# Optimization experiments

Measured on AMD Instinct MI355X. Metric: run time of the kernel, lower is better.

The kernel has to match this reference:

```python
import jax, jax.numpy as jnp
import numpy as np

B, N, T, F, H, HEADS, E, EDIM, P = 4, 1000, 8, 64, 64, 4, 16000, 16, 5
NEG_SLOPE = 0.2


def _seg_softmax(e, seg, n):
    # segment softmax over destination nodes; every segment is nonempty (self-loops)
    m = jax.ops.segment_max(e, seg, num_segments=n)
    ex = jnp.exp(e - m[seg])
    s = jax.ops.segment_sum(ex, seg, num_segments=n)
    return ex / s[seg]


def _gat(x, ei, W, a_src, a_dst, b):
    # PyG GATConv with concat=False (mean over heads), self-loops already in ei
    n = x.shape[0]
    heads, hh = a_src.shape
    h = (x @ W).reshape(n, heads, hh)                       # [N, heads, H]
    asrc = (h * a_src).sum(-1)                              # [N, heads]
    adst = (h * a_dst).sum(-1)
    src, dst = ei[0], ei[1]
    e = jax.nn.leaky_relu(asrc[src] + adst[dst], NEG_SLOPE)  # [E2, heads]
    alpha = _seg_softmax(e, dst, n)
    out = jax.ops.segment_sum(alpha[:, :, None] * h[src], dst, num_segments=n)
    return out.mean(1) + b                                   # [N, H]


def _gru_cell(x, h, Wih, Whh, bih, bhh):
    gi = x @ Wih.T + bih
    gh = h @ Whh.T + bhh
    i_r, i_z, i_n = jnp.split(gi, 3, axis=-1)
    h_r, h_z, h_n = jnp.split(gh, 3, axis=-1)
    r = jax.nn.sigmoid(i_r + h_r)
    z = jax.nn.sigmoid(i_z + h_z)
    nn_ = jnp.tanh(i_n + r * h_n)
    return (1.0 - z) * nn_ + z * h


def setup_inputs() -> dict:
    key = jax.random.key(0)
    ks = jax.random.split(key, 20)
    rn = lambda k, shp, s: (jax.random.normal(k, shp, jnp.float32) * s)
    inp = {}
    inp['x'] = jax.random.normal(ks[0], (B, N, T, F), jnp.float32)
    inp['edge_index_seq'] = jax.random.randint(ks[1], (B, T, 2, E), 0, N)
    inp['edge_feat_seq'] = jax.random.normal(ks[2], (B, T, E, EDIM), jnp.float32)
    inp['W1'] = rn(ks[3], (F, HEADS * H), 1 / np.sqrt(F))
    inp['att_src1'] = rn(ks[4], (HEADS, H), 1 / np.sqrt(H))
    inp['att_dst1'] = rn(ks[5], (HEADS, H), 1 / np.sqrt(H))
    inp['b1'] = jnp.zeros((H,), jnp.float32)
    inp['W2'] = rn(ks[6], (H, HEADS * H), 1 / np.sqrt(H))
    inp['att_src2'] = rn(ks[7], (HEADS, H), 1 / np.sqrt(H))
    inp['att_dst2'] = rn(ks[8], (HEADS, H), 1 / np.sqrt(H))
    inp['b2'] = jnp.zeros((H,), jnp.float32)
    inp['edge_W'] = rn(ks[9], (EDIM, H), 1 / np.sqrt(EDIM))
    inp['edge_b'] = jnp.zeros((H,), jnp.float32)
    inp['Wih0'] = rn(ks[10], (3 * H, H), 1 / np.sqrt(H))
    inp['Whh0'] = rn(ks[11], (3 * H, H), 1 / np.sqrt(H))
    inp['bih0'] = jnp.zeros((3 * H,), jnp.float32)
    inp['bhh0'] = jnp.zeros((3 * H,), jnp.float32)
    inp['Wih1'] = rn(ks[12], (3 * H, H), 1 / np.sqrt(H))
    inp['Whh1'] = rn(ks[13], (3 * H, H), 1 / np.sqrt(H))
    inp['bih1'] = jnp.zeros((3 * H,), jnp.float32)
    inp['bhh1'] = jnp.zeros((3 * H,), jnp.float32)
    inp['pW1'] = rn(ks[14], (H, H), 1 / np.sqrt(H))
    inp['pb1'] = jnp.zeros((H,), jnp.float32)
    inp['pW2'] = rn(ks[15], (H, 2 * P), 1 / np.sqrt(H))
    inp['pb2'] = jnp.zeros((2 * P,), jnp.float32)
    return inp


def reference(x, edge_index_seq, edge_feat_seq, W1, att_src1, att_dst1, b1,
              W2, att_src2, att_dst2, b2, edge_W, edge_b,
              Wih0, Whh0, bih0, bhh0, Wih1, Whh1, bih1, bhh1,
              pW1, pb1, pW2, pb2):
    Bs, Ns, Ts, Fs = x.shape
    G = Bs * Ts
    # [B,N,T,F] -> [B*T, N, F] (graph per (b,t))
    xg = x.transpose(0, 2, 1, 3).reshape(G, Ns, Fs)
    ei = edge_index_seq.reshape(G, 2, -1)
    # add self-loops (PyG GATConv default)
    sl = jnp.broadcast_to(jnp.arange(Ns), (G, 2, Ns))
    ei = jnp.concatenate([ei, sl], axis=-1)

    def per_graph(xt, e):
        h = jax.nn.relu(_gat(xt, e, W1, att_src1, att_dst1, b1))
        return _gat(h, e, W2, att_src2, att_dst2, b2)

    h = jax.vmap(per_graph)(xg, ei)                         # [G, N, H]
    Hd = h.shape[-1]
    # note: original computes edge_embedding(edge_feat) but never uses it (dead code)
    h = h.reshape(Bs, Ts, Ns, Hd).transpose(0, 2, 1, 3).reshape(Bs * Ns, Ts, Hd)
    xs = h.transpose(1, 0, 2)                               # [T, B*N, H]
    h0 = jnp.zeros((Bs * Ns, Hd), x.dtype)

    def step(carry, xt):
        h1, h2 = carry
        h1n = _gru_cell(xt, h1, Wih0, Whh0, bih0, bhh0)
        h2n = _gru_cell(h1n, h2, Wih1, Whh1, bih1, bhh1)
        return (h1n, h2n), None

    (_, hT), _ = jax.lax.scan(step, (h0, h0), xs)           # hT: [B*N, H]
    mid = jax.nn.relu(hT @ pW1 + pb1)
    pred = mid @ pW2 + pb2                                  # [B*N, 2P]
    return pred.reshape(Bs, Ns, P, 2)
```

## Files before the change

### kernel.cpp

```cpp
#include <hip/hip_runtime.h>
#include <math.h>

#define BB 4
#define NN 1000
#define TT 8
#define FF 64
#define HH 64
#define NHEADS 4
#define EE 16000
#define E2 17000
#define GG (BB*TT)
#define GN (GG*NN)
#define NROWS (BB*NN)

typedef __attribute__((ext_vector_type(8))) short bf16x8;
typedef __attribute__((ext_vector_type(4))) float f32x4;

__device__ __forceinline__ float sigmoidf_(float x) {
    return 1.f / (1.f + __expf(-x));
}
__device__ __forceinline__ float tanhf_(float x) {
    x = fminf(fmaxf(x, -15.f), 15.f);
    float e = __expf(2.f * x);
    return (e - 1.f) / (e + 1.f);
}
__device__ __forceinline__ float leaky_(float x) {
    return (x > 0.f) ? x : 0.2f * x;
}
__device__ __forceinline__ ushort bf16_rne(float v) {
    uint b = __float_as_uint(v);
    return (ushort)((b + 0x7FFF + ((b >> 16) & 1)) >> 16);
}

__global__ void count_edges(const int* __restrict__ ei, int* __restrict__ counts) {
    int g = blockIdx.y;
    int e = blockIdx.x * 256 + threadIdx.x;
    if (e >= E2) return;
    int dst;
    if (e < EE) dst = ei[(size_t)g * 2 * EE + EE + e];
    else        dst = e - EE;
    atomicAdd(&counts[g * NN + dst], 1);
}

__global__ __launch_bounds__(256) void scan_offsets_pg(const int* __restrict__ counts,
                                                       int* __restrict__ offs) {
    __shared__ int tot[256];
    int g = blockIdx.x;
    int tid = threadIdx.x;
    int base = tid * 4;
    int c0 = 0, c1 = 0, c2 = 0, c3 = 0;
    if (base < NN) {
        int4 v = *(const int4*)(counts + (size_t)g * NN + base);
        c0 = v.x; c1 = v.y; c2 = v.z; c3 = v.w;
    }
    int s = c0 + c1 + c2 + c3;
    tot[tid] = s;
    __syncthreads();
    for (int off = 1; off < 256; off <<= 1) {
        int y = (tid >= off) ? tot[tid - off] : 0;
        __syncthreads();
        tot[tid] += y;
        __syncthreads();
    }
    int run = g * E2 + tot[tid] - s;
    if (base < NN) {
        int4 o;
        o.x = run; run += c0;
        o.y = run; run += c1;
        o.z = run; run += c2;
        o.w = run;
        *(int4*)(offs + (size_t)g * NN + base) = o;
    }
    if (g == 0 && tid == 0) offs[GN] = GG * E2;
}

__global__ void scatter_edges(const int* __restrict__ ei, const int* __restrict__ offs,
                              int* __restrict__ cursor, int* __restrict__ csr) {
    int g = blockIdx.y;
    int e = blockIdx.x * 256 + threadIdx.x;
    if (e >= E2) return;
    int src, dst;
    if (e < EE) {
        src = ei[(size_t)g * 2 * EE + e];
        dst = ei[(size_t)g * 2 * EE + EE + e];
    } else {
        src = dst = e - EE;
    }
    int i = g * NN + dst;
    int pos = offs[i] + atomicAdd(&cursor[i], 1);
    csr[pos] = src;
}

#define PIN64_(arr)                                        \
    _Pragma("unroll")                                      \
    for (int _pi = 0; _pi < 64; ++_pi)                     \
        asm volatile("" : "+v"((arr)[_pi]));


template <int MODE>
__global__ __launch_bounds__(256) void xprep(
    const float* __restrict__ in, ushort* __restrict__ ap) {
    int g = blockIdx.x / 63, mt = blockIdx.x % 63;
    int tid = threadIdx.x;
    int xq = tid >> 7, kb = (tid >> 6) & 1, row = (tid >> 2) & 15, koct = tid & 3;
    int n = mt * 16 + row;
    int f0 = kb * 32 + koct * 8;
    float v[8];
    if (n < NN) {
        const float* xr;
        if (MODE == 0) {
            int b = g / TT, t = g % TT;
            xr = in + (((size_t)(b * NN + n) * TT + t) * FF);
        } else {
            xr = in + ((size_t)(g * NN + n) * FF);
        }
        float4 a = *(const float4*)(xr + f0);
        float4 c = *(const float4*)(xr + f0 + 4);
        v[0] = a.x; v[1] = a.y; v[2] = a.z; v[3] = a.w;
        v[4] = c.x; v[5] = c.y; v[6] = c.z; v[7] = c.w;
    } else {
#pragma unroll
        for (int j = 0; j < 8; ++j) v[j] = 0.f;
    }
    ushort o[8];
#pragma unroll
    for (int j = 0; j < 8; ++j) {
        ushort h = bf16_rne(v[j]);
        if (xq == 0) o[j] = h;
        else {
            float hf = __uint_as_float(((uint)h) << 16);
            o[j] = bf16_rne(v[j] - hf);
        }
    }
    size_t off = (size_t)(g * 63 + mt) * 2048
               + ((size_t)((xq * 2 + kb) * 16 + row) * 4 + koct) * 8;
    uint4 ow;
    ow.x = (uint)o[0] | ((uint)o[1] << 16);
    ow.y = (uint)o[2] | ((uint)o[3] << 16);
    ow.z = (uint)o[4] | ((uint)o[5] << 16);
    ow.w = (uint)o[6] | ((uint)o[7] << 16);
    *(uint4*)(ap + off) = ow;
}

__global__ __launch_bounds__(64) void wprep(
    const float* __restrict__ W1, const float* __restrict__ W2,
    ushort* __restrict__ B1, ushort* __restrict__ B2) {
    int blk = blockIdx.x;
    const float* W = (blk >> 6) ? W2 : W1;
    ushort* Bp = (blk >> 6) ? B2 : B1;
    int r = blk & 63;
    int wq = r >> 5, kb = (r >> 4) & 1, nt = r & 15;
    int tid = threadIdx.x;
    int col = tid >> 2, koct = tid & 3;
    int c = nt * 16 + col;
    ushort o[8];
#pragma unroll
    for (int j = 0; j < 8; ++j) {
        int k = kb * 32 + koct * 8 + j;
        float v = W[k * 256 + c];
        ushort h = bf16_rne(v);
        if (wq == 0) o[j] = h;
        else {
            float hf = __uint_as_float(((uint)h) << 16);
            o[j] = bf16_rne(v - hf);
        }
    }
    size_t off = (((size_t)((wq * 2 + kb) * 16 + nt) * 16 + col) * 4 + koct) * 8;
    uint4 ow;
    ow.x = (uint)o[0] | ((uint)o[1] << 16);
    ow.y = (uint)o[2] | ((uint)o[3] << 16);
    ow.z = (uint)o[4] | ((uint)o[5] << 16);
    ow.w = (uint)o[6] | ((uint)o[7] << 16);
    *(uint4*)(Bp + off) = ow;
}

__global__ __launch_bounds__(256) void gat_mfma(
    const ushort* __restrict__ ap, const ushort* __restrict__ bp,
    const float* __restrict__ att_s, const float* __restrict__ att_d,
    float* __restrict__ hlin, float* __restrict__ asrc, float* __restrict__ adst) {
    int g = blockIdx.x >> 4, band = blockIdx.x & 15;
    int tid = threadIdx.x;
    int w = tid >> 6, lane = tid & 63;
    int mt = band * 4 + w;
    if (mt >= 63) return;
    int lo = lane & 15, hi = lane >> 4;

    const ushort* abase = ap + (size_t)(g * 63 + mt) * 2048;
    size_t foff = ((size_t)(lo * 4 + hi)) * 8;
    bf16x8 Ah0 = *(const bf16x8*)(abase + 0 * 512 + foff);
    bf16x8 Ah1 = *(const bf16x8*)(abase + 1 * 512 + foff);
    bf16x8 Al0 = *(const bf16x8*)(abase + 2 * 512 + foff);
    bf16x8 Al1 = *(const bf16x8*)(abase + 3 * 512 + foff);

    f32x4 acc[16];
#pragma unroll
    for (int i = 0; i < 16; ++i) acc[i] = (f32x4){0.f, 0.f, 0.f, 0.f};

#pragma unroll
    for (int nt = 0; nt < 16; ++nt) {
        const ushort* bb = bp + (size_t)nt * 512 + foff;
        bf16x8 Bh0 = *(const bf16x8*)(bb + 0 * 8192);
        bf16x8 Bh1 = *(const bf16x8*)(bb + 1 * 8192);
        bf16x8 Bl0 = *(const bf16x8*)(bb + 2 * 8192);
        bf16x8 Bl1 = *(const bf16x8*)(bb + 3 * 8192);
        acc[nt] = __builtin_amdgcn_mfma_f32_16x16x32_bf16(Ah0, Bh0, acc[nt], 0, 0, 0);
        acc[nt] = __builtin_amdgcn_mfma_f32_16x16x32_bf16(Ah1, Bh1, acc[nt], 0, 0, 0);
        acc[nt] = __builtin_amdgcn_mfma_f32_16x16x32_bf16(Ah0, Bl0, acc[nt], 0, 0, 0);
        acc[nt] = __builtin_amdgcn_mfma_f32_16x16x32_bf16(Ah1, Bl1, acc[nt], 0, 0, 0);
        acc[nt] = __builtin_amdgcn_mfma_f32_16x16x32_bf16(Al0, Bh0, acc[nt], 0, 0, 0);
        acc[nt] = __builtin_amdgcn_mfma_f32_16x16x32_bf16(Al1, Bh1, acc[nt], 0, 0, 0);
        acc[nt] = __builtin_amdgcn_mfma_f32_16x16x32_bf16(Al0, Bl0, acc[nt], 0, 0, 0);
        acc[nt] = __builtin_amdgcn_mfma_f32_16x16x32_bf16(Al1, Bl1, acc[nt], 0, 0, 0);
    }

    float s1[4][4], s2[4][4];
#pragma unroll
    for (int r = 0; r < 4; ++r)
#pragma unroll
        for (int h = 0; h < 4; ++h) { s1[r][h] = 0.f; s2[r][h] = 0.f; }

#pragma unroll
    for (int nt = 0; nt < 16; ++nt) {
        int c = nt * 16 + lo;
        int head = nt >> 2;
        int slot = ((c & 63) << 2) + head;
        float as = att_s[c];
        float ad = att_d[c];
#pragma unroll
        for (int reg = 0; reg < 4; ++reg) {
            int n = mt * 16 + hi * 4 + reg;
            float v = acc[nt][reg];
            if (n < NN)
                hlin[((size_t)(g * NN + n) << 8) + slot] = v;
            s1[reg][head] += v * as;
            s2[reg][head] += v * ad;
        }
    }
#pragma unroll
    for (int off = 1; off < 16; off <<= 1) {
#pragma unroll
        for (int reg = 0; reg < 4; ++reg)
#pragma unroll
            for (int h = 0; h < 4; ++h) {
                s1[reg][h] += __shfl_xor(s1[reg][h], off, 64);
                s2[reg][h] += __shfl_xor(s2[reg][h], off, 64);
            }
    }
    if (lo == 0) {
#pragma unroll
        for (int reg = 0; reg < 4; ++reg) {
            int n = mt * 16 + hi * 4 + reg;
            if (n < NN) {
#pragma unroll
                for (int h = 0; h < 4; ++h) {
                    asrc[(size_t)(g * NN + n) * NHEADS + h] = s1[reg][h];
                    adst[(size_t)(g * NN + n) * NHEADS + h] = s2[reg][h];
                }
            }
        }
    }
}

__global__ __launch_bounds__(256) void gat_edge(
    const float* __restrict__ hlin, const float* __restrict__ asrc,
    const float* __restrict__ adst, const int* __restrict__ offs,
    const int* __restrict__ csr, const float* __restrict__ bias,
    float* __restrict__ out, int do_relu) {
    __shared__ float pbuf[4][64][4];
    __shared__ int   sbuf[4][64];
    __shared__ int   degs[4];
    int tid = threadIdx.x;
    int lane = tid & 63, w = tid >> 6;
    int B = blockIdx.x;
    int x = B & 7, j = B >> 3;
    int graph = x + 8 * (j / 250);
    int node = graph * NN + ((j % 250) << 2) + w;
    int beg = offs[node], end = offs[node + 1];
    int deg = end - beg;
    if (lane == 0) degs[w] = deg;
    __syncthreads();
    int maxdeg = max(max(degs[0], degs[1]), max(degs[2], degs[3]));
    int nchunk = (maxdeg + 63) >> 6;

    float4 ad = *(const float4*)(adst + (size_t)node * 4);
    const float* asrc_g = asrc + (size_t)graph * NN * 4;
    const float* hg = hlin + ((size_t)graph * NN << 8);

    float4 acc = make_float4(0.f, 0.f, 0.f, 0.f);
    float4 ssum = make_float4(0.f, 0.f, 0.f, 0.f);
    for (int c = 0; c < nchunk; ++c) {
        int e0 = beg + (c << 6);
        int myedge = e0 + lane;
        float4 p = make_float4(0.f, 0.f, 0.f, 0.f);
        int src = 0;
        if (myedge < end) {
            src = csr[myedge];
            float4 a = *(const float4*)(asrc_g + (size_t)src * 4);
            p.x = __expf(leaky_(a.x + ad.x));
            p.y = __expf(leaky_(a.y + ad.y));
            p.z = __expf(leaky_(a.z + ad.z));
            p.w = __expf(leaky_(a.w + ad.w));
        }
        float4 t = p;
#pragma unroll
        for (int off = 1; off < 64; off <<= 1) {
            t.x += __shfl_xor(t.x, off, 64);
            t.y += __shfl_xor(t.y, off, 64);
            t.z += __shfl_xor(t.z, off, 64);
            t.w += __shfl_xor(t.w, off, 64);
        }
        ssum.x += t.x; ssum.y += t.y; ssum.z += t.z; ssum.w += t.w;
        *(float4*)&pbuf[w][lane][0] = p;
        sbuf[w][lane] = src;
        __syncthreads();
        int cnt = end - e0;
        if (cnt > 64) cnt = 64;
        int cnt8 = (cnt + 7) & ~7;
        for (int e = 0; e < cnt8; e += 8) {
            float4 p0 = *(const float4*)&pbuf[w][e + 0][0];
            float4 p1 = *(const float4*)&pbuf[w][e + 1][0];
            float4 p2 = *(const float4*)&pbuf[w][e + 2][0];
            float4 p3 = *(const float4*)&pbuf[w][e + 3][0];
            float4 p4 = *(const float4*)&pbuf[w][e + 4][0];
            float4 p5 = *(const float4*)&pbuf[w][e + 5][0];
            float4 p6 = *(const float4*)&pbuf[w][e + 6][0];
            float4 p7 = *(const float4*)&pbuf[w][e + 7][0];
            int s0 = sbuf[w][e + 0], s1 = sbuf[w][e + 1];
            int s2 = sbuf[w][e + 2], s3 = sbuf[w][e + 3];
            int s4 = sbuf[w][e + 4], s5 = sbuf[w][e + 5];
            int s6 = sbuf[w][e + 6], s7 = sbuf[w][e + 7];
            int lo = lane << 2;
            float4 h0 = *(const float4*)(hg + (((size_t)s0) << 8) + lo);
            float4 h1 = *(const float4*)(hg + (((size_t)s1) << 8) + lo);
            float4 h2 = *(const float4*)(hg + (((size_t)s2) << 8) + lo);
            float4 h3 = *(const float4*)(hg + (((size_t)s3) << 8) + lo);
            float4 h4 = *(const float4*)(hg + (((size_t)s4) << 8) + lo);
            float4 h5 = *(const float4*)(hg + (((size_t)s5) << 8) + lo);
            float4 h6 = *(const float4*)(hg + (((size_t)s6) << 8) + lo);
            float4 h7 = *(const float4*)(hg + (((size_t)s7) << 8) + lo);
            acc.x = fmaf(p0.x, h0.x, acc.x); acc.y = fmaf(p0.y, h0.y, acc.y);
            acc.z = fmaf(p0.z, h0.z, acc.z); acc.w = fmaf(p0.w, h0.w, acc.w);
            acc.x = fmaf(p1.x, h1.x, acc.x); acc.y = fmaf(p1.y, h1.y, acc.y);
            acc.z = fmaf(p1.z, h1.z, acc.z); acc.w = fmaf(p1.w, h1.w, acc.w);
            acc.x = fmaf(p2.x, h2.x, acc.x); acc.y = fmaf(p2.y, h2.y, acc.y);
            acc.z = fmaf(p2.z, h2.z, acc.z); acc.w = fmaf(p2.w, h2.w, acc.w);
            acc.x = fmaf(p3.x, h3.x, acc.x); acc.y = fmaf(p3.y, h3.y, acc.y);
            acc.z = fmaf(p3.z, h3.z, acc.z); acc.w = fmaf(p3.w, h3.w, acc.w);
            acc.x = fmaf(p4.x, h4.x, acc.x); acc.y = fmaf(p4.y, h4.y, acc.y);
            acc.z = fmaf(p4.z, h4.z, acc.z); acc.w = fmaf(p4.w, h4.w, acc.w);
            acc.x = fmaf(p5.x, h5.x, acc.x); acc.y = fmaf(p5.y, h5.y, acc.y);
            acc.z = fmaf(p5.z, h5.z, acc.z); acc.w = fmaf(p5.w, h5.w, acc.w);
            acc.x = fmaf(p6.x, h6.x, acc.x); acc.y = fmaf(p6.y, h6.y, acc.y);
            acc.z = fmaf(p6.z, h6.z, acc.z); acc.w = fmaf(p6.w, h6.w, acc.w);
            acc.x = fmaf(p7.x, h7.x, acc.x); acc.y = fmaf(p7.y, h7.y, acc.y);
            acc.z = fmaf(p7.z, h7.z, acc.z); acc.w = fmaf(p7.w, h7.w, acc.w);
        }
        __syncthreads();
    }
    float o = 0.25f * (acc.x / ssum.x + acc.y / ssum.y + acc.z / ssum.z + acc.w / ssum.w)
            + bias[lane];
    if (do_relu) o = fmaxf(o, 0.f);
    out[((size_t)node << 6) + lane] = o;
}

template <int MODE>
__global__ __launch_bounds__(192, 4) void gru_gi(
    const float* __restrict__ in, const float* __restrict__ Wih,
    const float* __restrict__ bih, float* __restrict__ giseq) {
    const int ROWS = 10;
    int j = threadIdx.x;
    float wrow[64];
#pragma unroll
    for (int f4 = 0; f4 < 16; ++f4) {
        float4 w = *(const float4*)(Wih + (size_t)j * 64 + f4 * 4);
        wrow[4 * f4 + 0] = w.x; wrow[4 * f4 + 1] = w.y;
        wrow[4 * f4 + 2] = w.z; wrow[4 * f4 + 3] = w.w;
    }
    PIN64_(wrow)
    float bj = bih[j];
    int q0 = blockIdx.x * ROWS;
    int t = q0 / NROWS;
    int r0 = q0 - t * NROWS;
    for (int rr = 0; rr < ROWS; rr += 2) {
        const float *xa, *xb;
        if (MODE == 0) {
            int ra = r0 + rr, rb = ra + 1;
            int ba = ra / NN, na = ra - ba * NN;
            int bb2 = rb / NN, nb = rb - bb2 * NN;
            xa = in + (((size_t)(ba * TT + t) * NN + na) << 6);
            xb = in + (((size_t)(bb2 * TT + t) * NN + nb) << 6);
        } else {
            xa = in + ((size_t)(q0 + rr) << 6);
            xb = xa + 64;
        }
        float acca = bj, accb = bj;
#pragma unroll
        for (int f4 = 0; f4 < 16; ++f4) {
            float4 a4 = *(const float4*)(xa + f4 * 4);
            float4 b4 = *(const float4*)(xb + f4 * 4);
            acca = fmaf(a4.x, wrow[4 * f4 + 0], acca);
            acca = fmaf(a4.y, wrow[4 * f4 + 1], acca);
            acca = fmaf(a4.z, wrow[4 * f4 + 2], acca);
            acca = fmaf(a4.w, wrow[4 * f4 + 3], acca);
            accb = fmaf(b4.x, wrow[4 * f4 + 0], accb);
            accb = fmaf(b4.y, wrow[4 * f4 + 1], accb);
            accb = fmaf(b4.z, wrow[4 * f4 + 2], accb);
            accb = fmaf(b4.w, wrow[4 * f4 + 3], accb);
        }
        giseq[(size_t)(q0 + rr) * 192 + j] = acca;
        giseq[(size_t)(q0 + rr + 1) * 192 + j] = accb;
    }
}

template <int LAYER>
__global__ __launch_bounds__(128) void gru_rec(
    const float* __restrict__ giseq, const float* __restrict__ Whh,
    const float* __restrict__ bhh, float* __restrict__ outseq) {
    __shared__ float hs[4][64];
    int tid = threadIdx.x;
    int ch = tid & 63, w = tid >> 6;
    float wr[64], wz[64], wn[64];
#pragma unroll
    for (int k4 = 0; k4 < 16; ++k4) {
        float4 a = *(const float4*)(Whh + (size_t)ch * 64 + k4 * 4);
        float4 b = *(const float4*)(Whh + (size_t)(64 + ch) * 64 + k4 * 4);
        float4 c = *(const float4*)(Whh + (size_t)(128 + ch) * 64 + k4 * 4);
        wr[4*k4+0] = a.x; wr[4*k4+1] = a.y; wr[4*k4+2] = a.z; wr[4*k4+3] = a.w;
        wz[4*k4+0] = b.x; wz[4*k4+1] = b.y; wz[4*k4+2] = b.z; wz[4*k4+3] = b.w;
        wn[4*k4+0] = c.x; wn[4*k4+1] = c.y; wn[4*k4+2] = c.z; wn[4*k4+3] = c.w;
    }
    float br = bhh[ch], bz = bhh[64 + ch], bn = bhh[128 + ch];
    int row0 = blockIdx.x * 4 + w * 2;
    float hprev[2];
#pragma unroll
    for (int r = 0; r < 2; ++r) { hs[w * 2 + r][ch] = 0.f; hprev[r] = 0.f; }

    for (int t = 0; t < TT; ++t) {
#pragma unroll
        for (int r = 0; r < 2; ++r) {
            int row = row0 + r;
            const float* gp = giseq + ((size_t)(t * NROWS + row)) * 192;
            float gir = gp[ch], giz = gp[64 + ch], gin = gp[128 + ch];
            float ar = br, az = bz, an = bn;
#pragma unroll
            for (int k4 = 0; k4 < 16; ++k4) {
                float4 h4 = *(const float4*)&hs[w * 2 + r][k4 * 4];
                ar = fmaf(h4.x, wr[4*k4+0], ar); ar = fmaf(h4.y, wr[4*k4+1], ar);
                ar = fmaf(h4.z, wr[4*k4+2], ar); ar = fmaf(h4.w, wr[4*k4+3], ar);
                az = fmaf(h4.x, wz[4*k4+0], az); az = fmaf(h4.y, wz[4*k4+1], az);
                az = fmaf(h4.z, wz[4*k4+2], az); az = fmaf(h4.w, wz[4*k4+3], az);
                an = fmaf(h4.x, wn[4*k4+0], an); an = fmaf(h4.y, wn[4*k4+1], an);
                an = fmaf(h4.z, wn[4*k4+2], an); an = fmaf(h4.w, wn[4*k4+3], an);
            }
            float rg = sigmoidf_(gir + ar);
            float zg = sigmoidf_(giz + az);
            float ng = tanhf_(gin + rg * an);
            float hnew = (1.f - zg) * ng + zg * hprev[r];
            hprev[r] = hnew;
            hs[w * 2 + r][ch] = hnew;
            if (LAYER == 0)
                outseq[(((size_t)(t * NROWS + row)) << 6) + ch] = hnew;
        }
    }
    if (LAYER == 1) {
#pragma unroll
        for (int r = 0; r < 2; ++r)
            outseq[(((size_t)(row0 + r)) << 6) + ch] = hprev[r];
    }
}

__global__ __launch_bounds__(64) void mlp_head(
    const float* __restrict__ hT, const float* __restrict__ pW1,
    const float* __restrict__ pb1, const float* __restrict__ pW2,
    const float* __restrict__ pb2, float* __restrict__ out) {
    int r = blockIdx.x, lane = threadIdx.x;
    __shared__ float hrow[64];
    __shared__ float mid[64];
    hrow[lane] = hT[((size_t)r << 6) + lane];
    __syncthreads();
    float acc = pb1[lane];
#pragma unroll
    for (int k = 0; k < 64; ++k) acc = fmaf(hrow[k], pW1[k * 64 + lane], acc);
    mid[lane] = fmaxf(acc, 0.f);
    __syncthreads();
    if (lane < 10) {
        float o = pb2[lane];
#pragma unroll
        for (int k = 0; k < 64; ++k) o = fmaf(mid[k], pW2[k * 10 + lane], o);
        out[(size_t)r * 10 + lane] = o;
    }
}

extern "C" void kernel_launch(void* const* d_in, const int* in_sizes, int n_in,
                              void* d_out, int out_size, void* d_ws, size_t ws_size,
                              hipStream_t stream) {
    (void)in_sizes; (void)n_in; (void)out_size; (void)ws_size;
    const float* x    = (const float*)d_in[0];
    const int*   ei   = (const int*)d_in[1];
    const float* W1   = (const float*)d_in[3];
    const float* as1  = (const float*)d_in[4];
    const float* ad1  = (const float*)d_in[5];
    const float* b1   = (const float*)d_in[6];
    const float* W2   = (const float*)d_in[7];
    const float* as2  = (const float*)d_in[8];
    const float* ad2  = (const float*)d_in[9];
    const float* b2   = (const float*)d_in[10];
    const float* Wih0 = (const float*)d_in[13];
    const float* Whh0 = (const float*)d_in[14];
    const float* bih0 = (const float*)d_in[15];
    const float* bhh0 = (const float*)d_in[16];
    const float* Wih1 = (const float*)d_in[17];
    const float* Whh1 = (const float*)d_in[18];
    const float* bih1 = (const float*)d_in[19];
    const float* bhh1 = (const float*)d_in[20];
    const float* pW1  = (const float*)d_in[21];
    const float* pb1  = (const float*)d_in[22];
    const float* pW2  = (const float*)d_in[23];
    const float* pb2  = (const float*)d_in[24];
    float* out = (float*)d_out;

    char* ws = (char*)d_ws;
    float* hlin  = (float*)(ws + 0);
    float* giseq = hlin;
    float* asrc  = (float*)(ws + 32768000);
    float* hT    = asrc;
    float* adst  = (float*)(ws + 33280000);
    float* gat1  = (float*)(ws + 33792000);
    float* h1seq = gat1;
    float* gat2  = (float*)(ws + 41984000);
    ushort* Apack = (ushort*)(ws + 41984000);
    int* counts  = (int*)(ws + 50176000);
    int* cursor  = (int*)(ws + 50304000);
    int* offs    = (int*)(ws + 50432000);
    int* csr     = (int*)(ws + 50560256);
    ushort* Bp1  = (ushort*)(ws + 52736256);
    ushort* Bp2  = (ushort*)(ws + 52801792);

    hipMemsetAsync(counts, 0, 2 * GN * sizeof(int), stream);

    dim3 egrid((E2 + 255) / 256, GG);
    count_edges<<<egrid, 256, 0, stream>>>(ei, counts);
    scan_offsets_pg<<<GG, 256, 0, stream>>>(counts, offs);
    scatter_edges<<<egrid, 256, 0, stream>>>(ei, offs, cursor, csr);

    wprep<<<128, 64, 0, stream>>>(W1, W2, Bp1, Bp2);

    xprep<0><<<GG * 63, 256, 0, stream>>>(x, Apack);
    gat_mfma<<<GG * 16, 256, 0, stream>>>(Apack, Bp1, as1, ad1, hlin, asrc, adst);
    gat_edge<<<GN / 4, 256, 0, stream>>>(hlin, asrc, adst, offs, csr, b1, gat1, 1);
    xprep<1><<<GG * 63, 256, 0, stream>>>(gat1, Apack);
    gat_mfma<<<GG * 16, 256, 0, stream>>>(Apack, Bp2, as2, ad2, hlin, asrc, adst);
    gat_edge<<<GN / 4, 256, 0, stream>>>(hlin, asrc, adst, offs, csr, b2, gat2, 0);

    gru_gi<0><<<3200, 192, 0, stream>>>(gat2, Wih0, bih0, giseq);
    gru_rec<0><<<1000, 128, 0, stream>>>(giseq, Whh0, bhh0, h1seq);
    gru_gi<1><<<3200, 192, 0, stream>>>(h1seq, Wih1, bih1, giseq);
    gru_rec<1><<<1000, 128, 0, stream>>>(giseq, Whh1, bhh1, hT);

    mlp_head<<<NROWS, 64, 0, stream>>>(hT, pW1, pb1, pW2, pb2, out);
}
```

Measured before the change: 423.9 us.

## Fuse bf16 hi/lo input split into GAT MFMA kernel and split columns across waves

Removes the separate xprep pass that packed inputs into split bf16 hi/lo tiles; each GAT projection kernel now loads the fp32 rows directly and builds the A fragments in registers. The block grows to 512 threads so that two waves share each row tile, each computing half the output columns (two heads). This drops two kernel launches and the global round trip for the packed buffer, and halves the accumulator registers per wave. In exchange, the fp32 input is read by both wave halves, and the per-lane loads are less coalesced than the prepacked layout.

```diff
diff --git a/kernel.cpp b/kernel.cpp
--- a/kernel.cpp
+++ b/kernel.cpp
@@ -96,51 +96,6 @@
     for (int _pi = 0; _pi < 64; ++_pi)                     \
         asm volatile("" : "+v"((arr)[_pi]));
 
-
-template <int MODE>
-__global__ __launch_bounds__(256) void xprep(
-    const float* __restrict__ in, ushort* __restrict__ ap) {
-    int g = blockIdx.x / 63, mt = blockIdx.x % 63;
-    int tid = threadIdx.x;
-    int xq = tid >> 7, kb = (tid >> 6) & 1, row = (tid >> 2) & 15, koct = tid & 3;
-    int n = mt * 16 + row;
-    int f0 = kb * 32 + koct * 8;
-    float v[8];
-    if (n < NN) {
-        const float* xr;
-        if (MODE == 0) {
-            int b = g / TT, t = g % TT;
-            xr = in + (((size_t)(b * NN + n) * TT + t) * FF);
-        } else {
-            xr = in + ((size_t)(g * NN + n) * FF);
-        }
-        float4 a = *(const float4*)(xr + f0);
-        float4 c = *(const float4*)(xr + f0 + 4);
-        v[0] = a.x; v[1] = a.y; v[2] = a.z; v[3] = a.w;
-        v[4] = c.x; v[5] = c.y; v[6] = c.z; v[7] = c.w;
-    } else {
-#pragma unroll
-        for (int j = 0; j < 8; ++j) v[j] = 0.f;
-    }
-    ushort o[8];
-#pragma unroll
-    for (int j = 0; j < 8; ++j) {
-        ushort h = bf16_rne(v[j]);
-        if (xq == 0) o[j] = h;
-        else {
-            float hf = __uint_as_float(((uint)h) << 16);
-            o[j] = bf16_rne(v[j] - hf);
-        }
-    }
-    size_t off = (size_t)(g * 63 + mt) * 2048
-               + ((size_t)((xq * 2 + kb) * 16 + row) * 4 + koct) * 8;
-    uint4 ow;
-    ow.x = (uint)o[0] | ((uint)o[1] << 16);
-    ow.y = (uint)o[2] | ((uint)o[3] << 16);
-    ow.z = (uint)o[4] | ((uint)o[5] << 16);
-    ow.w = (uint)o[6] | ((uint)o[7] << 16);
-    *(uint4*)(ap + off) = ow;
-}
 
 __global__ __launch_bounds__(64) void wprep(
     const float* __restrict__ W1, const float* __restrict__ W2,
@@ -174,88 +129,119 @@
     *(uint4*)(Bp + off) = ow;
 }
 
-__global__ __launch_bounds__(256) void gat_mfma(
-    const ushort* __restrict__ ap, const ushort* __restrict__ bp,
+template <int MODE>
+__global__ __launch_bounds__(512, 4) void gat_mfma(
+    const float* __restrict__ in, const ushort* __restrict__ bp,
     const float* __restrict__ att_s, const float* __restrict__ att_d,
     float* __restrict__ hlin, float* __restrict__ asrc, float* __restrict__ adst) {
     int g = blockIdx.x >> 4, band = blockIdx.x & 15;
     int tid = threadIdx.x;
     int w = tid >> 6, lane = tid & 63;
-    int mt = band * 4 + w;
+    int mt = band * 4 + (w & 3);
+    int half = w >> 2;
     if (mt >= 63) return;
     int lo = lane & 15, hi = lane >> 4;
-
-    const ushort* abase = ap + (size_t)(g * 63 + mt) * 2048;
+    int n = mt * 16 + lo;
+
+    float xv[16];
+    if (n < NN) {
+        const float* xr;
+        if (MODE == 0) {
+            int b = g / TT, t = g % TT;
+            xr = in + (((size_t)(b * NN + n) * TT + t) * FF);
+        } else {
+            xr = in + ((size_t)(g * NN + n) * FF);
+        }
+        float4 a0 = *(const float4*)(xr + hi * 8);
+        float4 a1 = *(const float4*)(xr + hi * 8 + 4);
+        float4 b0 = *(const float4*)(xr + 32 + hi * 8);
+        float4 b1 = *(const float4*)(xr + 32 + hi * 8 + 4);
+        xv[0] = a0.x; xv[1] = a0.y; xv[2]  = a0.z; xv[3]  = a0.w;
+        xv[4] = a1.x; xv[5] = a1.y; xv[6]  = a1.z; xv[7]  = a1.w;
+        xv[8] = b0.x; xv[9] = b0.y; xv[10] = b0.z; xv[11] = b0.w;
+        xv[12] = b1.x; xv[13] = b1.y; xv[14] = b1.z; xv[15] = b1.w;
+    } else {
+#pragma unroll
+        for (int j = 0; j < 16; ++j) xv[j] = 0.f;
+    }
+    bf16x8 Ah0, Ah1, Al0, Al1;
+#pragma unroll
+    for (int j = 0; j < 8; ++j) {
+        ushort h0 = bf16_rne(xv[j]);
+        Ah0[j] = (short)h0;
+        Al0[j] = (short)bf16_rne(xv[j] - __uint_as_float(((uint)h0) << 16));
+        ushort h1 = bf16_rne(xv[8 + j]);
+        Ah1[j] = (short)h1;
+        Al1[j] = (short)bf16_rne(xv[8 + j] - __uint_as_float(((uint)h1) << 16));
+    }
+
     size_t foff = ((size_t)(lo * 4 + hi)) * 8;
-    bf16x8 Ah0 = *(const bf16x8*)(abase + 0 * 512 + foff);
-    bf16x8 Ah1 = *(const bf16x8*)(abase + 1 * 512 + foff);
-    bf16x8 Al0 = *(const bf16x8*)(abase + 2 * 512 + foff);
-    bf16x8 Al1 = *(const bf16x8*)(abase + 3 * 512 + foff);
-
-    f32x4 acc[16];
-#pragma unroll
-    for (int i = 0; i < 16; ++i) acc[i] = (f32x4){0.f, 0.f, 0.f, 0.f};
-
-#pragma unroll
-    for (int nt = 0; nt < 16; ++nt) {
+    f32x4 acc[8];
+#pragma unroll
+    for (int i = 0; i < 8; ++i) acc[i] = (f32x4){0.f, 0.f, 0.f, 0.f};
+
+#pragma unroll
+    for (int q = 0; q < 8; ++q) {
+        int nt = half * 8 + q;
         const ushort* bb = bp + (size_t)nt * 512 + foff;
         bf16x8 Bh0 = *(const bf16x8*)(bb + 0 * 8192);
         bf16x8 Bh1 = *(const bf16x8*)(bb + 1 * 8192);
         bf16x8 Bl0 = *(const bf16x8*)(bb + 2 * 8192);
         bf16x8 Bl1 = *(const bf16x8*)(bb + 3 * 8192);
-        acc[nt] = __builtin_amdgcn_mfma_f32_16x16x32_bf16(Ah0, Bh0, acc[nt], 0, 0, 0);
-        acc[nt] = __builtin_amdgcn_mfma_f32_16x16x32_bf16(Ah1, Bh1, acc[nt], 0, 0, 0);
-        acc[nt] = __builtin_amdgcn_mfma_f32_16x16x32_bf16(Ah0, Bl0, acc[nt], 0, 0, 0);
-        acc[nt] = __builtin_amdgcn_mfma_f32_16x16x32_bf16(Ah1, Bl1, acc[nt], 0, 0, 0);
-        acc[nt] = __builtin_amdgcn_mfma_f32_16x16x32_bf16(Al0, Bh0, acc[nt], 0, 0, 0);
-        acc[nt] = __builtin_amdgcn_mfma_f32_16x16x32_bf16(Al1, Bh1, acc[nt], 0, 0, 0);
-        acc[nt] = __builtin_amdgcn_mfma_f32_16x16x32_bf16(Al0, Bl0, acc[nt], 0, 0, 0);
-        acc[nt] = __builtin_amdgcn_mfma_f32_16x16x32_bf16(Al1, Bl1, acc[nt], 0, 0, 0);
-    }
-
-    float s1[4][4], s2[4][4];
-#pragma unroll
-    for (int r = 0; r < 4; ++r)
-#pragma unroll
-        for (int h = 0; h < 4; ++h) { s1[r][h] = 0.f; s2[r][h] = 0.f; }
-
-#pragma unroll
-    for (int nt = 0; nt < 16; ++nt) {
+        acc[q] = __builtin_amdgcn_mfma_f32_16x16x32_bf16(Ah0, Bh0, acc[q], 0, 0, 0);
+        acc[q] = __builtin_amdgcn_mfma_f32_16x16x32_bf16(Ah1, Bh1, acc[q], 0, 0, 0);
+        acc[q] = __builtin_amdgcn_mfma_f32_16x16x32_bf16(Ah0, Bl0, acc[q], 0, 0, 0);
+        acc[q] = __builtin_amdgcn_mfma_f32_16x16x32_bf16(Ah1, Bl1, acc[q], 0, 0, 0);
+        acc[q] = __builtin_amdgcn_mfma_f32_16x16x32_bf16(Al0, Bh0, acc[q], 0, 0, 0);
+        acc[q] = __builtin_amdgcn_mfma_f32_16x16x32_bf16(Al1, Bh1, acc[q], 0, 0, 0);
+        acc[q] = __builtin_amdgcn_mfma_f32_16x16x32_bf16(Al0, Bl0, acc[q], 0, 0, 0);
+        acc[q] = __builtin_amdgcn_mfma_f32_16x16x32_bf16(Al1, Bl1, acc[q], 0, 0, 0);
+    }
+
+    float s1[4][2], s2[4][2];
+#pragma unroll
+    for (int r = 0; r < 4; ++r) {
+        s1[r][0] = 0.f; s1[r][1] = 0.f;
+        s2[r][0] = 0.f; s2[r][1] = 0.f;
+    }
+#pragma unroll
+    for (int q = 0; q < 8; ++q) {
+        int nt = half * 8 + q;
         int c = nt * 16 + lo;
         int head = nt >> 2;
+        int hh = q >> 2;
         int slot = ((c & 63) << 2) + head;
         float as = att_s[c];
         float ad = att_d[c];
 #pragma unroll
         for (int reg = 0; reg < 4; ++reg) {
-            int n = mt * 16 + hi * 4 + reg;
-            float v = acc[nt][reg];
-            if (n < NN)
-                hlin[((size_t)(g * NN + n) << 8) + slot] = v;
-            s1[reg][head] += v * as;
-            s2[reg][head] += v * ad;
+            int nr = mt * 16 + hi * 4 + reg;
+            float v = acc[q][reg];
+            if (nr < NN)
+                hlin[((size_t)(g * NN + nr) << 8) + slot] = v;
+            s1[reg][hh] += v * as;
+            s2[reg][hh] += v * ad;
         }
     }
 #pragma unroll
     for (int off = 1; off < 16; off <<= 1) {
 #pragma unroll
-        for (int reg = 0; reg < 4; ++reg)
-#pragma unroll
-            for (int h = 0; h < 4; ++h) {
-                s1[reg][h] += __shfl_xor(s1[reg][h], off, 64);
-                s2[reg][h] += __shfl_xor(s2[reg][h], off, 64);
-            }
+        for (int reg = 0; reg < 4; ++reg) {
+            s1[reg][0] += __shfl_xor(s1[reg][0], off, 64);
+            s1[reg][1] += __shfl_xor(s1[reg][1], off, 64);
+            s2[reg][0] += __shfl_xor(s2[reg][0], off, 64);
+            s2[reg][1] += __shfl_xor(s2[reg][1], off, 64);
+        }
     }
     if (lo == 0) {
 #pragma unroll
         for (int reg = 0; reg < 4; ++reg) {
-            int n = mt * 16 + hi * 4 + reg;
-            if (n < NN) {
-#pragma unroll
-                for (int h = 0; h < 4; ++h) {
-                    asrc[(size_t)(g * NN + n) * NHEADS + h] = s1[reg][h];
-                    adst[(size_t)(g * NN + n) * NHEADS + h] = s2[reg][h];
-                }
+            int nr = mt * 16 + hi * 4 + reg;
+            if (nr < NN) {
+                asrc[(size_t)(g * NN + nr) * NHEADS + half * 2 + 0] = s1[reg][0];
+                asrc[(size_t)(g * NN + nr) * NHEADS + half * 2 + 1] = s1[reg][1];
+                adst[(size_t)(g * NN + nr) * NHEADS + half * 2 + 0] = s2[reg][0];
+                adst[(size_t)(g * NN + nr) * NHEADS + half * 2 + 1] = s2[reg][1];
             }
         }
     }
@@ -528,7 +514,6 @@
     float* gat1  = (float*)(ws + 33792000);
     float* h1seq = gat1;
     float* gat2  = (float*)(ws + 41984000);
-    ushort* Apack = (ushort*)(ws + 41984000);
     int* counts  = (int*)(ws + 50176000);
     int* cursor  = (int*)(ws + 50304000);
     int* offs    = (int*)(ws + 50432000);
@@ -545,11 +530,9 @@
 
     wprep<<<128, 64, 0, stream>>>(W1, W2, Bp1, Bp2);
 
-    xprep<0><<<GG * 63, 256, 0, stream>>>(x, Apack);
-    gat_mfma<<<GG * 16, 256, 0, stream>>>(Apack, Bp1, as1, ad1, hlin, asrc, adst);
+    gat_mfma<0><<<GG * 16, 512, 0, stream>>>(x, Bp1, as1, ad1, hlin, asrc, adst);
     gat_edge<<<GN / 4, 256, 0, stream>>>(hlin, asrc, adst, offs, csr, b1, gat1, 1);
-    xprep<1><<<GG * 63, 256, 0, stream>>>(gat1, Apack);
-    gat_mfma<<<GG * 16, 256, 0, stream>>>(Apack, Bp2, as2, ad2, hlin, asrc, adst);
+    gat_mfma<1><<<GG * 16, 512, 0, stream>>>(gat1, Bp2, as2, ad2, hlin, asrc, adst);
     gat_edge<<<GN / 4, 256, 0, stream>>>(hlin, asrc, adst, offs, csr, b2, gat2, 0);
 
     gru_gi<0><<<3200, 192, 0, stream>>>(gat2, Wih0, bih0, giseq);
```

After: 409.9 us. 1.03x faster.
